# Optimization experiments

Hardware: AMD Instinct MI355X
Metric: run time of the kernel (lower is better)

The kernel has to match this reference:

```python
import jax, jax.numpy as jnp
import numpy as np

RADIUS = 0.1
KSIZE = 3          # kernel points per dimension
P_DIM = 3
K = KSIZE ** P_DIM  # 27 kernel points
KP_EXTENT = RADIUS / (KSIZE - 1) * P_DIM ** 0.5


def _kernel_points():
    # grid kernel points, same as getKernelPoints(radius, 3, dim=3)
    xyz = np.linspace(-1.0, 1.0, KSIZE)
    pts = np.meshgrid(*P_DIM * [xyz])
    pts = np.vstack([p.flatten() for p in pts]).T
    pts = pts / P_DIM ** 0.5
    return jnp.asarray(pts * RADIUS, dtype=jnp.float32)  # [K, 3]


def setup_inputs() -> dict:
    key = jax.random.key(0)
    k1, k2, k3, k4, k5 = jax.random.split(key, 5)
    N, S, H, CIN, COUT = 40000, 40000, 32, 64, 64
    # points in a [0, 0.2]^3 cube so neighbor offsets are comparable to radius
    q_pts = jax.random.uniform(k1, (N, 3), jnp.float32) * 0.2
    s_pts = jax.random.uniform(k2, (S, 3), jnp.float32) * 0.2
    neighb_inds = jax.random.randint(k3, (N, H), 0, S)
    x = jax.random.normal(k4, (S, CIN), jnp.float32)
    # kaiming-style init for the [K, Cin, Cout] grouped weights
    weights = jax.random.normal(k5, (K, CIN, COUT), jnp.float32) * (1.0 / np.sqrt(CIN))
    return {"q_pts": q_pts, "s_pts": s_pts, "neighb_inds": neighb_inds,
            "x": x, "weights": weights}


def reference(q_pts, s_pts, neighb_inds, x, weights):
    kp = _kernel_points()  # [K, 3], non-trainable constant
    # shadow padding row (sentinel point far away, zero feature)
    s_pad = jnp.concatenate([s_pts, jnp.full((1, s_pts.shape[-1]), 1e6, s_pts.dtype)], axis=0)
    x_pad = jnp.concatenate([x, jnp.zeros((1, x.shape[-1]), x.dtype)], axis=0)
    neighbors = s_pad[neighb_inds] - q_pts[:, None, :]      # [N, H, 3]
    neighb_x = x_pad[neighb_inds]                           # [N, H, Cin]
    # kernel-point influence weights: linear correlation clipped at 0
    diff = neighbors[:, :, None, :] - kp[None, None, :, :]  # [N, H, K, 3]
    sq_dist = jnp.sum(diff * diff, axis=-1)                 # [N, H, K]
    all_w = jnp.maximum(1.0 - jnp.sqrt(sq_dist) / KP_EXTENT, 0.0)
    # weighted grouped matmul over K kernel weight matrices
    fx = jnp.einsum('nhl,nhi,lio->no', all_w, neighb_x, weights)  # [N, Cout]
    return fx
```

## Files before the change

### kernel.cpp

```cpp
#include <hip/hip_runtime.h>

typedef _Float16 half_t;
typedef __fp16   fp16x2 __attribute__((ext_vector_type(2)));
typedef _Float16 half4_t __attribute__((ext_vector_type(4)));
typedef _Float16 half8   __attribute__((ext_vector_type(8)));
typedef float    f32x4   __attribute__((ext_vector_type(4)));
typedef unsigned short u16x8 __attribute__((ext_vector_type(8)));

#define KP_S    0.057735026918962574f
#define INV_EXT 11.547005383792515f
#define NTILE   2500
#define WT_BYTES (64 * 1792 * 2)
#define XH_BYTES (40000 * 64 * 2)
#define G_BYTES  (40000 * 3584)
#define TROW     57344

#define GPITCH  3616
#define NBLK_F  512

union H8 { half8 v; fp16x2 h2[4]; };
union H4 { half4_t v; fp16x2 h2[2]; };


__global__ void build_pre(const float* __restrict__ W, const float* __restrict__ x,
                          half_t* __restrict__ WT, half_t* __restrict__ xh) {
    if (blockIdx.x < 448) {
        int t = blockIdx.x * 256 + threadIdx.x;
        int o = t / 1792, k = t - o * 1792;
        int l, i;
        if (k < 1024) {
            int nt = k >> 8, m = (k >> 2) & 63, r = k & 3;
            l = 4 * (m >> 4) + r;  i = 16 * nt + (m & 15);
        } else {
            int u = k - 1024;
            int nt = u / 192, v = u - nt * 192;
            int m = v >> 2, r = v & 3;
            l = 16 + 4 * (m >> 4) + r;  i = 16 * nt + (m & 15);
        }
        int c = 4 * (i & 15) + (i >> 4);
        WT[(k >> 5) * 2048 + o * 32 + (k & 31)] = (half_t)W[(l * 64 + c) * 64 + o];
    } else {
        int t = (blockIdx.x - 448) * 256 + threadIdx.x;
        f32x4 v = *(const f32x4*)(x + t * 4);
        H4 h;
        h.h2[0] = __builtin_amdgcn_cvt_pkrtz(v.x, v.y);
        h.h2[1] = __builtin_amdgcn_cvt_pkrtz(v.z, v.w);
        *(half4_t*)(xh + t * 4) = h.v;
    }
}

__global__ void build_wt_fused(const float* __restrict__ W, half_t* __restrict__ WT) {
    int t = blockIdx.x * 256 + threadIdx.x;
    if (t >= 64 * 1792) return;
    int o = t / 1792, k = t - o * 1792;
    int i = k / 28,   l = k - i * 28;
    int c = 4 * (i & 15) + (i >> 4);
    WT[t] = (l < 27) ? (half_t)W[(l * 64 + c) * 64 + o] : (half_t)0.f;
}

__global__ void build_xh(const float* __restrict__ x, half_t* __restrict__ xh) {
    int t = blockIdx.x * 256 + threadIdx.x;
    f32x4 v = *(const f32x4*)(x + t * 4);
    H4 h;
    h.h2[0] = __builtin_amdgcn_cvt_pkrtz(v.x, v.y);
    h.h2[1] = __builtin_amdgcn_cvt_pkrtz(v.z, v.w);
    *(half4_t*)(xh + t * 4) = h.v;
}

__global__ __launch_bounds__(512, 6) void kpconvA(
    const float* __restrict__ q_pts, const float* __restrict__ s_pts,
    const int*   __restrict__ inds,  const half_t* __restrict__ xh,
    half_t* __restrict__ G)
{
    __shared__ __align__(16) unsigned short idx_lds[16][32];
    __shared__ __align__(16) f32x4 nbr_lds[16][32];

    const int tid  = threadIdx.x;
    const int lane = tid & 63, wid = tid >> 6;
    const int lr   = lane & 15, g = lane >> 4;
    const int aq   = tid >> 5,  ah = tid & 31;
    const int base = blockIdx.x * 16;
    char* gt = (char*)G + (size_t)blockIdx.x * TROW;

    const float kx0 = (float)((lr / 3) % 3 - 1) * KP_S;
    const float ky0 = (float)( lr / 9      - 1) * KP_S;
    const float kz0 = (float)( lr % 3      - 1) * KP_S;
    const int   l1  = lr + 16;
    const float kx1 = (float)((l1 / 3) % 3 - 1) * KP_S;
    const float ky1 = (float)( l1 / 9      - 1) * KP_S;
    const float kz1 = (float)( l1 % 3      - 1) * KP_S;
    const float cbias = (l1 < 27) ? 1.f : -1.f;

    {
        int n   = base + aq;
        int idx = inds[n * 32 + ah];
        idx_lds[aq][ah] = (unsigned short)idx;
        f32x4 v;
        v.x = s_pts[idx * 3 + 0] - q_pts[n * 3 + 0];
        v.y = s_pts[idx * 3 + 1] - q_pts[n * 3 + 1];
        v.z = s_pts[idx * 3 + 2] - q_pts[n * 3 + 2];
        v.w = 0.f;
        nbr_lds[aq][ah] = v;
    }
    __syncthreads();

    half4_t xvA[8], xvB[8];
    {
        u16x8 idA = *(const u16x8*)&idx_lds[2 * wid][8 * g];
        u16x8 idB = *(const u16x8*)&idx_lds[2 * wid + 1][8 * g];
        #pragma unroll
        for (int j = 0; j < 8; ++j) {
            xvA[j] = *(const half4_t*)(xh + (int)idA[j] * 64 + 4 * lr);
            xvB[j] = *(const half4_t*)(xh + (int)idB[j] * 64 + 4 * lr);
        }
    }

    const int so0 = (lane >> 3) * 1024 + (lane & 7) * 8;
    #pragma unroll
    for (int qq = 0; qq < 2; ++qq) {
        const int q = 2 * wid + qq;
        float w0v[8], w1v[8];
        #pragma unroll
        for (int j = 0; j < 8; ++j) {
            f32x4 nb = nbr_lds[q][8 * g + j];
            float dx = nb.x - kx0, dy = nb.y - ky0, dz = nb.z - kz0;
            w0v[j] = fmaxf(fmaf(__builtin_amdgcn_sqrtf(dx*dx + dy*dy + dz*dz), -INV_EXT, 1.f), 0.f);
            float ex = nb.x - kx1, ey = nb.y - ky1, ez = nb.z - kz1;
            w1v[j] = fmaxf(fmaf(__builtin_amdgcn_sqrtf(ex*ex + ey*ey + ez*ez), -INV_EXT, cbias), 0.f);
        }
        H8 A0, A1;
        #pragma unroll
        for (int p = 0; p < 4; ++p) {
            A0.h2[p] = __builtin_amdgcn_cvt_pkrtz(w0v[2*p], w0v[2*p+1]);
            A1.h2[p] = __builtin_amdgcn_cvt_pkrtz(w1v[2*p], w1v[2*p+1]);
        }
        #pragma unroll
        for (int nt = 0; nt < 4; ++nt) {
            half8 b;
            #pragma unroll
            for (int j = 0; j < 8; ++j) b[j] = (qq ? xvB : xvA)[j][nt];
            f32x4 z = {0.f, 0.f, 0.f, 0.f};
            f32x4 c0 = __builtin_amdgcn_mfma_f32_16x16x32_f16(A0.v, b, z, 0, 0, 0);
            f32x4 c1 = __builtin_amdgcn_mfma_f32_16x16x32_f16(A1.v, b, z, 0, 0, 0);
            H4 h0;
            h0.h2[0] = __builtin_amdgcn_cvt_pkrtz(c0[0], c0[1]);
            h0.h2[1] = __builtin_amdgcn_cvt_pkrtz(c0[2], c0[3]);
            __builtin_nontemporal_store(h0.v, (half4_t*)(gt + nt * 8192 + so0 + q * 64));
            if (lane < 48) {
                H4 h1;
                h1.h2[0] = __builtin_amdgcn_cvt_pkrtz(c1[0], c1[1]);
                h1.h2[1] = __builtin_amdgcn_cvt_pkrtz(c1[2], c1[3]);
                __builtin_nontemporal_store(h1.v, (half4_t*)(gt + 32768 + nt * 6144 + so0 + q * 64));
            }
        }
    }
}

__global__ __launch_bounds__(256, 4) void kpconvB(
    const half_t* __restrict__ G, const half_t* __restrict__ WT,
    float* __restrict__ out)
{
    __shared__ __align__(16) f32x4 red[3][2][4][64];

    const int tid  = threadIdx.x;
    const int lane = tid & 63, kq = tid >> 6;
    const int lr   = lane & 15, g = lane >> 4;
    const int T0   = blockIdx.x * 2;

    const char* ga0 = (const char*)G + (size_t)T0 * TROW + kq * 14336 + lr * 64 + g * 16;
    const char* ga1 = ga0 + TROW;
    const char* wb  = (const char*)WT + kq * 57344 + lr * 64 + g * 16;

    f32x4 a00 = {0,0,0,0}, a01 = {0,0,0,0}, a02 = {0,0,0,0}, a03 = {0,0,0,0};
    f32x4 a10 = {0,0,0,0}, a11 = {0,0,0,0}, a12 = {0,0,0,0}, a13 = {0,0,0,0};

    #pragma unroll
    for (int s = 0; s < 14; ++s) {
        half8 av0 = *(const half8*)(ga0 + s * 1024);
        half8 av1 = *(const half8*)(ga1 + s * 1024);
        half8 b0  = *(const half8*)(wb + s * 4096);
        half8 b1  = *(const half8*)(wb + s * 4096 + 1024);
        half8 b2  = *(const half8*)(wb + s * 4096 + 2048);
        half8 b3  = *(const half8*)(wb + s * 4096 + 3072);
        a00 = __builtin_amdgcn_mfma_f32_16x16x32_f16(av0, b0, a00, 0, 0, 0);
        a01 = __builtin_amdgcn_mfma_f32_16x16x32_f16(av0, b1, a01, 0, 0, 0);
        a02 = __builtin_amdgcn_mfma_f32_16x16x32_f16(av0, b2, a02, 0, 0, 0);
        a03 = __builtin_amdgcn_mfma_f32_16x16x32_f16(av0, b3, a03, 0, 0, 0);
        a10 = __builtin_amdgcn_mfma_f32_16x16x32_f16(av1, b0, a10, 0, 0, 0);
        a11 = __builtin_amdgcn_mfma_f32_16x16x32_f16(av1, b1, a11, 0, 0, 0);
        a12 = __builtin_amdgcn_mfma_f32_16x16x32_f16(av1, b2, a12, 0, 0, 0);
        a13 = __builtin_amdgcn_mfma_f32_16x16x32_f16(av1, b3, a13, 0, 0, 0);
    }

    if (kq) {
        *(f32x4*)&red[kq - 1][0][0][lane] = a00;
        *(f32x4*)&red[kq - 1][0][1][lane] = a01;
        *(f32x4*)&red[kq - 1][0][2][lane] = a02;
        *(f32x4*)&red[kq - 1][0][3][lane] = a03;
        *(f32x4*)&red[kq - 1][1][0][lane] = a10;
        *(f32x4*)&red[kq - 1][1][1][lane] = a11;
        *(f32x4*)&red[kq - 1][1][2][lane] = a12;
        *(f32x4*)&red[kq - 1][1][3][lane] = a13;
    }
    __syncthreads();
    if (kq == 0) {
        f32x4 r0[4] = {a00, a01, a02, a03};
        f32x4 r1[4] = {a10, a11, a12, a13};
        #pragma unroll
        for (int j = 0; j < 4; ++j) {
            #pragma unroll
            for (int p = 0; p < 3; ++p) {
                r0[j] += red[p][0][j][lane];
                r1[j] += red[p][1][j][lane];
            }
        }
        #pragma unroll
        for (int r = 0; r < 4; ++r) {
            float* o0 = out + (T0 * 16 + 4 * g + r) * 64 + lr;
            float* o1 = out + ((T0 + 1) * 16 + 4 * g + r) * 64 + lr;
            #pragma unroll
            for (int j = 0; j < 4; ++j) {
                o0[16 * j] = r0[j][r];
                o1[16 * j] = r1[j][r];
            }
        }
    }
}


#define ISSUE_XV1(BUF, Q, XV) do {                                             \
    u16x8 id8 = *(const u16x8*)&idx_lds[BUF][Q][8 * g];                        \
    _Pragma("unroll")                                                          \
    for (int j = 0; j < 8; ++j) {                                              \
        if constexpr (XHALF) {                                                 \
            XV[j] = *(const half4_t*)(xh + (int)id8[j] * 64 + 4 * lr);         \
        } else {                                                               \
            f32x4 t4 = *(const f32x4*)(x + (int)id8[j] * 64 + 4 * lr);         \
            H4 hh;                                                             \
            hh.h2[0] = __builtin_amdgcn_cvt_pkrtz(t4.x, t4.y);                 \
            hh.h2[1] = __builtin_amdgcn_cvt_pkrtz(t4.z, t4.w);                 \
            XV[j] = hh.v;                                                      \
        }                                                                      \
    }                                                                          \
} while (0)

#define PACK_B(XV, BF) do {                                                    \
    _Pragma("unroll")                                                          \
    for (int nt = 0; nt < 4; ++nt) {                                           \
        half8 b;                                                               \
        _Pragma("unroll")                                                      \
        for (int j = 0; j < 8; ++j) b[j] = XV[j][nt];                          \
        BF[nt].v = b;                                                          \
    }                                                                          \
} while (0)

#define MFMA_DUMP(Q, CUR, BF) do {                                             \
    float w0v[8], w1v[8];                                                      \
    _Pragma("unroll")                                                          \
    for (int j = 0; j < 8; ++j) {                                              \
        f32x4 nb = nbr_lds[CUR][Q][8 * g + j];                                 \
        float dx = nb.x - kx0, dy = nb.y - ky0, dz = nb.z - kz0;               \
        w0v[j] = fmaxf(fmaf(__builtin_amdgcn_sqrtf(dx*dx + dy*dy + dz*dz), -INV_EXT, 1.f), 0.f); \
        float ex = nb.x - kx1, ey = nb.y - ky1, ez = nb.z - kz1;               \
        w1v[j] = fmaxf(fmaf(__builtin_amdgcn_sqrtf(ex*ex + ey*ey + ez*ez), -INV_EXT, cbias), 0.f); \
    }                                                                          \
    H8 A0, A1;                                                                 \
    _Pragma("unroll")                                                          \
    for (int p = 0; p < 4; ++p) {                                              \
        A0.h2[p] = __builtin_amdgcn_cvt_pkrtz(w0v[2*p], w0v[2*p+1]);           \
        A1.h2[p] = __builtin_amdgcn_cvt_pkrtz(w1v[2*p], w1v[2*p+1]);           \
    }                                                                          \
    char* gq = g_mem + (Q) * GPITCH;                                           \
    _Pragma("unroll")                                                          \
    for (int nt = 0; nt < 4; ++nt) {                                           \
        f32x4 z = {0.f, 0.f, 0.f, 0.f};                                        \
        f32x4 c0 = __builtin_amdgcn_mfma_f32_16x16x32_f16(A0.v, BF[nt].v, z, 0, 0, 0); \
        f32x4 c1 = __builtin_amdgcn_mfma_f32_16x16x32_f16(A1.v, BF[nt].v, z, 0, 0, 0); \
        const int ic = 16 * nt + lr;                                           \
        H4 h0;                                                                 \
        h0.h2[0] = __builtin_amdgcn_cvt_pkrtz(c0[0], c0[1]);                   \
        h0.h2[1] = __builtin_amdgcn_cvt_pkrtz(c0[2], c0[3]);                   \
        *(half4_t*)(gq + 2 * (ic * 28 + 4 * g)) = h0.v;                        \
        if (4 * g < 12) {                                                      \
            H4 h1;                                                             \
            h1.h2[0] = __builtin_amdgcn_cvt_pkrtz(c1[0], c1[1]);               \
            h1.h2[1] = __builtin_amdgcn_cvt_pkrtz(c1[2], c1[3]);               \
            *(half4_t*)(gq + 2 * (ic * 28 + 16 + 4 * g)) = h1.v;               \
        }                                                                      \
    }                                                                          \
} while (0)

#define BODY(T, TN, CUR, XV) do {                                              \
    half4_t xvB[8];                                                            \
    ISSUE_XV1(CUR, 2 * wid + 1, xvB);                                          \
    H8 BFA[4];                                                                 \
    PACK_B(XV, BFA);                                                           \
    const int nn   = (TN) * 16 + aq;                                           \
    const int idxN = inds[nn * 32 + ah];                                       \
    MFMA_DUMP(2 * wid, CUR, BFA);                                              \
    f32x4 vN;                                                                  \
    vN.x = s_pts[idxN * 3 + 0] - q_pts[nn * 3 + 0];                            \
    vN.y = s_pts[idxN * 3 + 1] - q_pts[nn * 3 + 1];                            \
    vN.z = s_pts[idxN * 3 + 2] - q_pts[nn * 3 + 2];                            \
    vN.w = 0.f;                                                                \
    H8 BFB[4];                                                                 \
    PACK_B(xvB, BFB);                                                          \
    MFMA_DUMP(2 * wid + 1, CUR, BFB);                                          \
    idx_lds[(CUR) ^ 1][aq][ah] = (unsigned short)idxN;                         \
    nbr_lds[(CUR) ^ 1][aq][ah] = vN;                                           \
    __syncthreads();                                                           \
    ISSUE_XV1((CUR) ^ 1, 2 * wid, XV);                                         \
    const half_t* wrow = WT + (16 * ot + lr) * 1792 + kh * 896 + 8 * g;        \
    const char*   gb   = g_mem + lr * GPITCH + kh * 1792;                      \
    f32x4 accA = {0.f, 0.f, 0.f, 0.f}, accB = {0.f, 0.f, 0.f, 0.f};            \
    _Pragma("unroll 7")                                                        \
    for (int s = 0; s < 28; s += 2) {                                          \
        half8 aA = *(const half8*)(gb + 64 * s + 16 * g);                      \
        half8 bA = *(const half8*)(wrow + 32 * s);                             \
        accA = __builtin_amdgcn_mfma_f32_16x16x32_f16(aA, bA, accA, 0, 0, 0);  \
        half8 aB = *(const half8*)(gb + 64 * (s + 1) + 16 * g);                \
        half8 bB = *(const half8*)(wrow + 32 * (s + 1));                       \
        accB = __builtin_amdgcn_mfma_f32_16x16x32_f16(aB, bB, accB, 0, 0, 0);  \
    }                                                                          \
    f32x4 acc = accA + accB;                                                   \
    if (kh) *(f32x4*)&red[ot][lane] = acc;                                     \
    __syncthreads();                                                           \
    if (!kh) {                                                                 \
        f32x4 p = red[ot][lane];                                               \
        const int o = 16 * ot + lr;                                            \
        _Pragma("unroll")                                                      \
        for (int r = 0; r < 4; ++r)                                            \
            out[((T) * 16 + 4 * g + r) * 64 + o] = acc[r] + p[r];              \
    }                                                                          \
} while (0)

template <int XHALF>
__global__ __launch_bounds__(512, 4) void kpconv_fused(
    const float* __restrict__ q_pts, const float* __restrict__ s_pts,
    const int*   __restrict__ inds,  const float* __restrict__ x,
    const half_t* __restrict__ xh,   const half_t* __restrict__ WT,
    float* __restrict__ out)
{
    __shared__ __align__(16) char   g_mem[16 * GPITCH];
    __shared__ __align__(16) unsigned short idx_lds[2][16][32];
    __shared__ __align__(16) f32x4  nbr_lds[2][16][32];
    __shared__ __align__(16) f32x4  red[4][64];

    const int tid  = threadIdx.x;
    const int lane = tid & 63, wid = tid >> 6;
    const int lr   = lane & 15, g = lane >> 4;
    const int aq   = tid >> 5,  ah = tid & 31;
    const int ot   = wid & 3,   kh = wid >> 2;

    const float kx0 = (float)((lr / 3) % 3 - 1) * KP_S;
    const float ky0 = (float)( lr / 9      - 1) * KP_S;
    const float kz0 = (float)( lr % 3      - 1) * KP_S;
    const int   l1  = lr + 16;
    const float kx1 = (float)((l1 / 3) % 3 - 1) * KP_S;
    const float ky1 = (float)( l1 / 9      - 1) * KP_S;
    const float kz1 = (float)( l1 % 3      - 1) * KP_S;
    const float cbias = (l1 < 27) ? 1.f : -1.f;

    {
        int n   = blockIdx.x * 16 + aq;
        int idx = inds[n * 32 + ah];
        idx_lds[0][aq][ah] = (unsigned short)idx;
        f32x4 v;
        v.x = s_pts[idx * 3 + 0] - q_pts[n * 3 + 0];
        v.y = s_pts[idx * 3 + 1] - q_pts[n * 3 + 1];
        v.z = s_pts[idx * 3 + 2] - q_pts[n * 3 + 2];
        v.w = 0.f;
        nbr_lds[0][aq][ah] = v;
    }
    __syncthreads();

    half4_t xv[8];
    ISSUE_XV1(0, 2 * wid, xv);

    int cur = 0;
    for (int t = blockIdx.x; t < NTILE; t += NBLK_F) {
        int tn = (t + NBLK_F < NTILE) ? t + NBLK_F : t;
        BODY(t, tn, cur, xv);
        cur ^= 1;
    }
}


extern "C" void kernel_launch(void* const* d_in, const int* in_sizes, int n_in,
                              void* d_out, int out_size, void* d_ws, size_t ws_size,
                              hipStream_t stream) {
    const float* q_pts = (const float*)d_in[0];
    const float* s_pts = (const float*)d_in[1];
    const int*   inds  = (const int*)d_in[2];
    const float* x     = (const float*)d_in[3];
    const float* W     = (const float*)d_in[4];
    float* out = (float*)d_out;
    half_t* WT = (half_t*)d_ws;
    half_t* xh = (half_t*)((char*)d_ws + WT_BYTES);
    half_t* G  = (half_t*)((char*)d_ws + WT_BYTES + XH_BYTES);

    const size_t need_split = (size_t)WT_BYTES + XH_BYTES + G_BYTES;
    const size_t need_xh    = (size_t)WT_BYTES + XH_BYTES;

    if (ws_size >= need_split) {
        build_pre<<<2948, 256, 0, stream>>>(W, x, WT, xh);
        kpconvA<<<2500, 512, 0, stream>>>(q_pts, s_pts, inds, xh, G);
        kpconvB<<<1250, 256, 0, stream>>>(G, WT, out);
    } else if (ws_size >= need_xh) {
        build_wt_fused<<<448, 256, 0, stream>>>(W, WT);
        build_xh<<<2500, 256, 0, stream>>>(x, xh);
        kpconv_fused<1><<<NBLK_F, 512, 0, stream>>>(q_pts, s_pts, inds, x, xh, WT, out);
    } else {
        build_wt_fused<<<448, 256, 0, stream>>>(W, WT);
        kpconv_fused<0><<<NBLK_F, 512, 0, stream>>>(q_pts, s_pts, inds, x, xh, WT, out);
    }
}
```

Baseline: 88.52 us.

## Make kpconvA persistent with double-buffered LDS prefetch of next tile's neighbors

kpconvA now runs a fixed grid of 768 blocks that loop over the 2500 tiles instead of launching one block per tile. While the current tile's kernel-point weights are computed, each block gathers the next tile's neighbor indices and offsets into a second LDS buffer, then crosses a barrier and swaps buffers. The aim is to hide gather latency and cut block launch and prologue cost. In exchange it adds a barrier per tile, doubles LDS use and raises register pressure. 2500 tiles over 768 blocks leaves the last round unevenly loaded.

```diff
diff --git a/kernel.cpp b/kernel.cpp
--- a/kernel.cpp
+++ b/kernel.cpp
@@ -10,6 +10,7 @@
 #define KP_S    0.057735026918962574f
 #define INV_EXT 11.547005383792515f
 #define NTILE   2500
+#define NBLKA   768
 #define WT_BYTES (64 * 1792 * 2)
 #define XH_BYTES (40000 * 64 * 2)
 #define G_BYTES  (40000 * 3584)
@@ -20,6 +21,11 @@
 
 union H8 { half8 v; fp16x2 h2[4]; };
 union H4 { half4_t v; fp16x2 h2[2]; };
+
+#define BAR_LGKM() do {                                                        \
+    __asm__ volatile("s_waitcnt lgkmcnt(0)\n\ts_barrier" ::: "memory");        \
+    __builtin_amdgcn_sched_barrier(0);                                         \
+} while (0)
 
 
 __global__ void build_pre(const float* __restrict__ W, const float* __restrict__ x,
@@ -72,15 +78,13 @@
     const int*   __restrict__ inds,  const half_t* __restrict__ xh,
     half_t* __restrict__ G)
 {
-    __shared__ __align__(16) unsigned short idx_lds[16][32];
-    __shared__ __align__(16) f32x4 nbr_lds[16][32];
+    __shared__ __align__(16) unsigned short idx_lds[2][16][32];
+    __shared__ __align__(16) f32x4 nbr_lds[2][16][32];
 
     const int tid  = threadIdx.x;
     const int lane = tid & 63, wid = tid >> 6;
     const int lr   = lane & 15, g = lane >> 4;
     const int aq   = tid >> 5,  ah = tid & 31;
-    const int base = blockIdx.x * 16;
-    char* gt = (char*)G + (size_t)blockIdx.x * TROW;
 
     const float kx0 = (float)((lr / 3) % 3 - 1) * KP_S;
     const float ky0 = (float)( lr / 9      - 1) * KP_S;
@@ -92,67 +96,95 @@
     const float cbias = (l1 < 27) ? 1.f : -1.f;
 
     {
-        int n   = base + aq;
+        int n   = blockIdx.x * 16 + aq;
         int idx = inds[n * 32 + ah];
-        idx_lds[aq][ah] = (unsigned short)idx;
+        idx_lds[0][aq][ah] = (unsigned short)idx;
         f32x4 v;
         v.x = s_pts[idx * 3 + 0] - q_pts[n * 3 + 0];
         v.y = s_pts[idx * 3 + 1] - q_pts[n * 3 + 1];
         v.z = s_pts[idx * 3 + 2] - q_pts[n * 3 + 2];
         v.w = 0.f;
-        nbr_lds[aq][ah] = v;
+        nbr_lds[0][aq][ah] = v;
     }
     __syncthreads();
 
-    half4_t xvA[8], xvB[8];
-    {
-        u16x8 idA = *(const u16x8*)&idx_lds[2 * wid][8 * g];
-        u16x8 idB = *(const u16x8*)&idx_lds[2 * wid + 1][8 * g];
+    const int so0 = (lane >> 3) * 1024 + (lane & 7) * 8;
+    int cur = 0;
+    for (int t = blockIdx.x; t < NTILE; t += NBLKA) {
+        char* gt = (char*)G + (size_t)t * TROW;
+
+        half4_t xvA[8], xvB[8];
+        {
+            u16x8 idA = *(const u16x8*)&idx_lds[cur][2 * wid][8 * g];
+            u16x8 idB = *(const u16x8*)&idx_lds[cur][2 * wid + 1][8 * g];
+            #pragma unroll
+            for (int j = 0; j < 8; ++j) {
+                xvA[j] = *(const half4_t*)(xh + (int)idA[j] * 64 + 4 * lr);
+                xvB[j] = *(const half4_t*)(xh + (int)idB[j] * 64 + 4 * lr);
+            }
+        }
+
+        const int tn   = (t + NBLKA < NTILE) ? t + NBLKA : t;
+        const int nn   = tn * 16 + aq;
+        const int idxN = inds[nn * 32 + ah];
+        f32x4 vN;
+        vN.x = s_pts[idxN * 3 + 0] - q_pts[nn * 3 + 0];
+        vN.y = s_pts[idxN * 3 + 1] - q_pts[nn * 3 + 1];
+        vN.z = s_pts[idxN * 3 + 2] - q_pts[nn * 3 + 2];
+        vN.w = 0.f;
+
+        H8 A0a, A1a, A0b, A1b;
         #pragma unroll
-        for (int j = 0; j < 8; ++j) {
-            xvA[j] = *(const half4_t*)(xh + (int)idA[j] * 64 + 4 * lr);
-            xvB[j] = *(const half4_t*)(xh + (int)idB[j] * 64 + 4 * lr);
-        }
-    }
-
-    const int so0 = (lane >> 3) * 1024 + (lane & 7) * 8;
-    #pragma unroll
-    for (int qq = 0; qq < 2; ++qq) {
-        const int q = 2 * wid + qq;
-        float w0v[8], w1v[8];
+        for (int qq = 0; qq < 2; ++qq) {
+            const int q = 2 * wid + qq;
+            float w0v[8], w1v[8];
+            #pragma unroll
+            for (int j = 0; j < 8; ++j) {
+                f32x4 nb = nbr_lds[cur][q][8 * g + j];
+                float dx = nb.x - kx0, dy = nb.y - ky0, dz = nb.z - kz0;
+                w0v[j] = fmaxf(fmaf(__builtin_amdgcn_sqrtf(dx*dx + dy*dy + dz*dz), -INV_EXT, 1.f), 0.f);
+                float ex = nb.x - kx1, ey = nb.y - ky1, ez = nb.z - kz1;
+                w1v[j] = fmaxf(fmaf(__builtin_amdgcn_sqrtf(ex*ex + ey*ey + ez*ez), -INV_EXT, cbias), 0.f);
+            }
+            H8* A0 = qq ? &A0b : &A0a;
+            H8* A1 = qq ? &A1b : &A1a;
+            #pragma unroll
+            for (int p = 0; p < 4; ++p) {
+                A0->h2[p] = __builtin_amdgcn_cvt_pkrtz(w0v[2*p], w0v[2*p+1]);
+                A1->h2[p] = __builtin_amdgcn_cvt_pkrtz(w1v[2*p], w1v[2*p+1]);
+            }
+        }
+
+        idx_lds[cur ^ 1][aq][ah] = (unsigned short)idxN;
+        nbr_lds[cur ^ 1][aq][ah] = vN;
+
         #pragma unroll
-        for (int j = 0; j < 8; ++j) {
-            f32x4 nb = nbr_lds[q][8 * g + j];
-            float dx = nb.x - kx0, dy = nb.y - ky0, dz = nb.z - kz0;
-            w0v[j] = fmaxf(fmaf(__builtin_amdgcn_sqrtf(dx*dx + dy*dy + dz*dz), -INV_EXT, 1.f), 0.f);
-            float ex = nb.x - kx1, ey = nb.y - ky1, ez = nb.z - kz1;
-            w1v[j] = fmaxf(fmaf(__builtin_amdgcn_sqrtf(ex*ex + ey*ey + ez*ez), -INV_EXT, cbias), 0.f);
-        }
-        H8 A0, A1;
-        #pragma unroll
-        for (int p = 0; p < 4; ++p) {
-            A0.h2[p] = __builtin_amdgcn_cvt_pkrtz(w0v[2*p], w0v[2*p+1]);
-            A1.h2[p] = __builtin_amdgcn_cvt_pkrtz(w1v[2*p], w1v[2*p+1]);
-        }
-        #pragma unroll
-        for (int nt = 0; nt < 4; ++nt) {
-            half8 b;
-            #pragma unroll
-            for (int j = 0; j < 8; ++j) b[j] = (qq ? xvB : xvA)[j][nt];
-            f32x4 z = {0.f, 0.f, 0.f, 0.f};
-            f32x4 c0 = __builtin_amdgcn_mfma_f32_16x16x32_f16(A0.v, b, z, 0, 0, 0);
-            f32x4 c1 = __builtin_amdgcn_mfma_f32_16x16x32_f16(A1.v, b, z, 0, 0, 0);
-            H4 h0;
-            h0.h2[0] = __builtin_amdgcn_cvt_pkrtz(c0[0], c0[1]);
-            h0.h2[1] = __builtin_amdgcn_cvt_pkrtz(c0[2], c0[3]);
-            __builtin_nontemporal_store(h0.v, (half4_t*)(gt + nt * 8192 + so0 + q * 64));
-            if (lane < 48) {
-                H4 h1;
-                h1.h2[0] = __builtin_amdgcn_cvt_pkrtz(c1[0], c1[1]);
-                h1.h2[1] = __builtin_amdgcn_cvt_pkrtz(c1[2], c1[3]);
-                __builtin_nontemporal_store(h1.v, (half4_t*)(gt + 32768 + nt * 6144 + so0 + q * 64));
-            }
-        }
+        for (int qq = 0; qq < 2; ++qq) {
+            const int q = 2 * wid + qq;
+            const H8& A0 = qq ? A0b : A0a;
+            const H8& A1 = qq ? A1b : A1a;
+            #pragma unroll
+            for (int nt = 0; nt < 4; ++nt) {
+                half8 b;
+                #pragma unroll
+                for (int j = 0; j < 8; ++j) b[j] = (qq ? xvB : xvA)[j][nt];
+                f32x4 z = {0.f, 0.f, 0.f, 0.f};
+                f32x4 c0 = __builtin_amdgcn_mfma_f32_16x16x32_f16(A0.v, b, z, 0, 0, 0);
+                f32x4 c1 = __builtin_amdgcn_mfma_f32_16x16x32_f16(A1.v, b, z, 0, 0, 0);
+                H4 h0;
+                h0.h2[0] = __builtin_amdgcn_cvt_pkrtz(c0[0], c0[1]);
+                h0.h2[1] = __builtin_amdgcn_cvt_pkrtz(c0[2], c0[3]);
+                __builtin_nontemporal_store(h0.v, (half4_t*)(gt + nt * 8192 + so0 + q * 64));
+                if (lane < 48) {
+                    H4 h1;
+                    h1.h2[0] = __builtin_amdgcn_cvt_pkrtz(c1[0], c1[1]);
+                    h1.h2[1] = __builtin_amdgcn_cvt_pkrtz(c1[2], c1[3]);
+                    __builtin_nontemporal_store(h1.v, (half4_t*)(gt + 32768 + nt * 6144 + so0 + q * 64));
+                }
+            }
+        }
+        BAR_LGKM();
+        cur ^= 1;
     }
 }
 
@@ -404,7 +436,7 @@
 
     if (ws_size >= need_split) {
         build_pre<<<2948, 256, 0, stream>>>(W, x, WT, xh);
-        kpconvA<<<2500, 512, 0, stream>>>(q_pts, s_pts, inds, xh, G);
+        kpconvA<<<NBLKA, 512, 0, stream>>>(q_pts, s_pts, inds, xh, G);
         kpconvB<<<1250, 256, 0, stream>>>(G, WT, out);
     } else if (ws_size >= need_xh) {
         build_wt_fused<<<448, 256, 0, stream>>>(W, WT);
```

New measurement: 153.2 us. +73.1%, slower.
